# Performance work log

Measured on AMD Instinct MI355X. Metric: run time of the kernel, lower is better.

The kernel has to match this reference:

```python
import jax, jax.numpy as jnp
import numpy as np

N = 100000      # num zones (nodes)
E = 1600000     # num edges
IN = 16         # in_channels
HID = 128       # hidden_dim
HEADS = 4
C = HID // HEADS  # 32, per-head channels of gat1
NEG = 0.2       # PyG GATConv negative_slope default
LN_EPS = 1e-5


def setup_inputs() -> dict:
    key = jax.random.key(0)
    ks = jax.random.split(key, 14)
    x = jax.random.normal(ks[0], (N, IN), jnp.float32)
    edge_index = jax.random.randint(ks[1], (2, E), 0, N, dtype=jnp.int32)
    # --- GATConv layer 1: in=IN, heads=HEADS, out=C, concat=True ---
    W1 = jax.random.normal(ks[2], (IN, HEADS * C), jnp.float32) / np.sqrt(IN)
    a_src1 = jax.random.normal(ks[3], (HEADS, C), jnp.float32) / np.sqrt(C)
    a_dst1 = jax.random.normal(ks[4], (HEADS, C), jnp.float32) / np.sqrt(C)
    b1 = jnp.zeros((HEADS * C,), jnp.float32)
    # --- LayerNorm 1 ---
    g1 = jnp.ones((HID,), jnp.float32)
    beta1 = jnp.zeros((HID,), jnp.float32)
    # --- GATConv layer 2: in=HID, heads=1, out=HID, concat=False ---
    W2 = jax.random.normal(ks[5], (HID, HID), jnp.float32) / np.sqrt(HID)
    a_src2 = jax.random.normal(ks[6], (1, HID), jnp.float32) / np.sqrt(HID)
    a_dst2 = jax.random.normal(ks[7], (1, HID), jnp.float32) / np.sqrt(HID)
    b2 = jnp.zeros((HID,), jnp.float32)
    # --- LayerNorm 2 ---
    g2 = jnp.ones((HID,), jnp.float32)
    beta2 = jnp.zeros((HID,), jnp.float32)
    return dict(x=x, edge_index=edge_index, W1=W1, a_src1=a_src1, a_dst1=a_dst1,
                b1=b1, g1=g1, beta1=beta1, W2=W2, a_src2=a_src2, a_dst2=a_dst2,
                b2=b2, g2=g2, beta2=beta2)


def gat_conv(x, src, dst, W, a_src, a_dst, b, heads, ch, concat):
    """PyG GATConv (eval mode, no edge_attr), self-loops already in src/dst."""
    n = x.shape[0]
    h = (x @ W).reshape(n, heads, ch)                    # [N,H,C]
    alpha_src = jnp.einsum('nhc,hc->nh', h, a_src)       # [N,H]
    alpha_dst = jnp.einsum('nhc,hc->nh', h, a_dst)       # [N,H]
    e = jax.nn.leaky_relu(alpha_src[src] + alpha_dst[dst], NEG)  # [Etot,H]
    # segment softmax over destination node
    m = jax.ops.segment_max(e, dst, num_segments=n)      # [N,H]
    ex = jnp.exp(e - m[dst])
    denom = jax.ops.segment_sum(ex, dst, num_segments=n) # [N,H]
    alpha = ex / denom[dst]                              # [Etot,H]
    msg = h[src] * alpha[..., None]                      # [Etot,H,C]
    out = jax.ops.segment_sum(msg, dst, num_segments=n)  # [N,H,C]
    out = out.reshape(n, heads * ch) if concat else out.mean(axis=1)
    return out + b


def layer_norm(x, g, b):
    mu = x.mean(-1, keepdims=True)
    var = ((x - mu) ** 2).mean(-1, keepdims=True)
    return (x - mu) * jax.lax.rsqrt(var + LN_EPS) * g + b


def reference(x, edge_index, W1, a_src1, a_dst1, b1, g1, beta1,
              W2, a_src2, a_dst2, b2, g2, beta2):
    loops = jnp.arange(N, dtype=edge_index.dtype)
    src = jnp.concatenate([edge_index[0], loops])
    dst = jnp.concatenate([edge_index[1], loops])
    h = gat_conv(x, src, dst, W1, a_src1, a_dst1, b1, HEADS, C, concat=True)
    h = layer_norm(jax.nn.elu(h), g1, beta1)
    h = gat_conv(h, src, dst, W2, a_src2, a_dst2, b2, 1, HID, concat=False)
    h = layer_norm(jax.nn.elu(h), g2, beta2)
    return h
```

## Files before the change

### kernel.cpp

```cpp
#include <hip/hip_runtime.h>

#define IN_CH 16
#define HID 128
#define HEADS 4
#define NEG 0.2f
#define LN_EPS 1e-5f
#define BCAP 8192

typedef short bf16x8 __attribute__((ext_vector_type(8)));
typedef float f32x4 __attribute__((ext_vector_type(4)));

__device__ __forceinline__ float bf2f(unsigned short u) {
  return __uint_as_float(((unsigned)u) << 16);
}
__device__ __forceinline__ float bflo(unsigned u) {
  return __uint_as_float(u << 16);
}
__device__ __forceinline__ float bfhi(unsigned u) {
  return __uint_as_float(u & 0xffff0000u);
}
__device__ __forceinline__ unsigned short f2bf(float f) {
  unsigned u = __float_as_uint(f);
  unsigned r = (u + 0x7fffu + ((u >> 16) & 1u)) >> 16;
  return (unsigned short)r;
}
__device__ __forceinline__ float sb(unsigned v, int sh) {
  return (float)((int)(v << (24 - sh)) >> 24);
}

__global__ __launch_bounds__(256) void k_gemm1(
    const float* __restrict__ x, const float* __restrict__ W1,
    const float* __restrict__ a_src, const float* __restrict__ a_dst,
    signed char* __restrict__ hq, float* __restrict__ rec,
    float* __restrict__ adst, int N) {
  __shared__ float w1s[IN_CH][HID];
  __shared__ float xsh[8][IN_CH];
  int tid = threadIdx.x;
  int nb = blockIdx.x * 8;
  for (int i = tid; i < IN_CH * HID; i += 256) ((float*)w1s)[i] = W1[i];
  if (tid < 128) {
    int nl = tid >> 4, k = tid & 15;
    int n = nb + nl;
    xsh[nl][k] = (n < N) ? x[n * IN_CH + k] : 0.f;
  }
  __syncthreads();
  int nl = tid >> 5;
  int l32 = tid & 31;
  int c0 = l32 << 2;
  int n = nb + nl;
  float4 acc = make_float4(0.f, 0.f, 0.f, 0.f);
#pragma unroll
  for (int k = 0; k < IN_CH; ++k) {
    float xv = xsh[nl][k];
    float4 wv = *(const float4*)(&w1s[k][c0]);
    acc.x += xv * wv.x;
    acc.y += xv * wv.y;
    acc.z += xv * wv.z;
    acc.w += xv * wv.w;
  }
  float4 as4 = *(const float4*)(a_src + c0);
  float4 ad4 = *(const float4*)(a_dst + c0);
  float av = acc.x * as4.x + acc.y * as4.y + acc.z * as4.z + acc.w * as4.w;
  float dv = acc.x * ad4.x + acc.y * ad4.y + acc.z * ad4.z + acc.w * ad4.w;
  av += __shfl_xor(av, 1);
  av += __shfl_xor(av, 2);
  av += __shfl_xor(av, 4);
  dv += __shfl_xor(dv, 1);
  dv += __shfl_xor(dv, 2);
  dv += __shfl_xor(dv, 4);
  float m = fmaxf(fmaxf(fabsf(acc.x), fabsf(acc.y)),
                  fmaxf(fabsf(acc.z), fabsf(acc.w)));
#pragma unroll
  for (int o = 1; o < 32; o <<= 1) m = fmaxf(m, __shfl_xor(m, o));
  if (n < N) {
    float rs = (m > 0.f) ? 127.f / m : 0.f;
    int b0 = __float2int_rn(acc.x * rs) & 255;
    int b1 = __float2int_rn(acc.y * rs) & 255;
    int b2 = __float2int_rn(acc.z * rs) & 255;
    int b3 = __float2int_rn(acc.w * rs) & 255;
    *(unsigned*)(hq + (size_t)n * HID + c0) =
        (unsigned)(b0 | (b1 << 8) | (b2 << 16) | (b3 << 24));
    if ((l32 & 7) == 0) {
      rec[n * 8 + (l32 >> 3)] = av;
      adst[n * HEADS + (l32 >> 3)] = dv;
    }
    if (l32 == 0) rec[n * 8 + 4] = m * (1.f / 127.f);
  }
}

__global__ __launch_bounds__(256) void k_hist(
    const int* __restrict__ ei, int E, int Etot, int NBK, int NBLK,
    int* __restrict__ bcnt) {
  __shared__ int lh[512];
  int blk = blockIdx.x;
  for (int i = threadIdx.x; i < 512; i += 256) lh[i] = 0;
  __syncthreads();
  int s0 = blk * 8192, s1 = min(s0 + 8192, Etot);
  for (int e = s0 + threadIdx.x; e < s1; e += 256) {
    int d = (e < E) ? ei[E + e] : (e - E);
    atomicAdd(&lh[d >> 8], 1);
  }
  __syncthreads();
  for (int i = threadIdx.x; i < NBK; i += 256) bcnt[i * NBLK + blk] = lh[i];
}

__global__ __launch_bounds__(256) void k_scan1(
    const int* __restrict__ deg, int* __restrict__ part, int* __restrict__ aux,
    int N) {
  int i = blockIdx.x * 256 + threadIdx.x;
  int v = (i < N) ? deg[i] : 0;
  int lane = threadIdx.x & 63, w = threadIdx.x >> 6;
  int inc = v;
#pragma unroll
  for (int o = 1; o < 64; o <<= 1) {
    int t = __shfl_up(inc, o, 64);
    if (lane >= o) inc += t;
  }
  __shared__ int wsum[4];
  if (lane == 63) wsum[w] = inc;
  __syncthreads();
  int woff = 0;
#pragma unroll
  for (int k = 0; k < 4; ++k)
    if (k < w) woff += wsum[k];
  if (i < N) part[i] = woff + inc - v;
  if (threadIdx.x == 255) aux[blockIdx.x] = woff + inc;
}

__global__ __launch_bounds__(512) void k_scan2(int* __restrict__ aux, int nb) {
  int i = threadIdx.x;
  int v = (i < nb) ? aux[i] : 0;
  int lane = i & 63, w = i >> 6;
  int inc = v;
#pragma unroll
  for (int o = 1; o < 64; o <<= 1) {
    int t = __shfl_up(inc, o, 64);
    if (lane >= o) inc += t;
  }
  __shared__ int wsum[8];
  if (lane == 63) wsum[w] = inc;
  __syncthreads();
  int woff = 0;
#pragma unroll
  for (int k = 0; k < 8; ++k)
    if (k < w) woff += wsum[k];
  if (i < nb) aux[i] = woff + inc - v;
}

__global__ __launch_bounds__(256) void k_scan3g(
    const int* __restrict__ part, const int* __restrict__ aux,
    int* __restrict__ out, int M) {
  int i = blockIdx.x * 256 + threadIdx.x;
  if (i < M) out[i] = part[i] + aux[blockIdx.x];
}

__global__ __launch_bounds__(256) void k_bucket(
    const int* __restrict__ ei, const int* __restrict__ bpre, int E, int Etot,
    int NBK, int NBLK, unsigned* __restrict__ bbuf) {
  __shared__ int lc[512];
  int blk = blockIdx.x;
  for (int i = threadIdx.x; i < NBK; i += 256) lc[i] = bpre[i * NBLK + blk];
  __syncthreads();
  int s0 = blk * 8192, s1 = min(s0 + 8192, Etot);
  for (int e = s0 + threadIdx.x; e < s1; e += 256) {
    int d = (e < E) ? ei[E + e] : (e - E);
    int s = (e < E) ? ei[e] : d;
    int pos = atomicAdd(&lc[d >> 8], 1);
    bbuf[pos] = ((unsigned)s << 8) | (unsigned)(d & 255);
  }
}

__global__ __launch_bounds__(256) void k_build(
    const unsigned* __restrict__ bbuf, const int* __restrict__ bpre,
    int* __restrict__ rowstart, int* __restrict__ csr_src, int N, int Etot,
    int NBK, int NBLK) {
  __shared__ int ldeg[256], lcur[256], wsum[4];
  __shared__ int lout[BCAP];
  int bin = blockIdx.x;
  int base = bpre[bin * NBLK];
  int next = (bin + 1 < NBK) ? bpre[(bin + 1) * NBLK] : Etot;
  int cnt = next - base;
  if (cnt > BCAP) cnt = BCAP;
  int tid = threadIdx.x;
  ldeg[tid] = 0;
  __syncthreads();
  for (int i = tid; i < cnt; i += 256)
    atomicAdd(&ldeg[bbuf[base + i] & 255u], 1);
  __syncthreads();
  int v = ldeg[tid];
  int lane = tid & 63, wv = tid >> 6;
  int inc = v;
#pragma unroll
  for (int o = 1; o < 64; o <<= 1) {
    int t = __shfl_up(inc, o, 64);
    if (lane >= o) inc += t;
  }
  if (lane == 63) wsum[wv] = inc;
  __syncthreads();
  int woff = 0;
#pragma unroll
  for (int k = 0; k < 4; ++k)
    if (k < wv) woff += wsum[k];
  int pre = woff + inc - v;
  int node = bin * 256 + tid;
  if (node < N) rowstart[node] = base + pre;
  lcur[tid] = pre;
  __syncthreads();
  for (int i = tid; i < cnt; i += 256) {
    unsigned u = bbuf[base + i];
    int p = atomicAdd(&lcur[u & 255u], 1);
    lout[p] = (int)(u >> 8);
  }
  __syncthreads();
  for (int i = tid; i < cnt; i += 256) csr_src[base + i] = lout[i];
  if (bin == 0 && tid == 0) rowstart[N] = Etot;
}

__global__ __launch_bounds__(256) void k_agg1(
    const int* __restrict__ rowstart, const int* __restrict__ csr_src,
    const float* __restrict__ rec, const float* __restrict__ adst,
    const signed char* __restrict__ hq, const float* __restrict__ bias,
    const float* __restrict__ g, const float* __restrict__ beta,
    unsigned short* __restrict__ outb, int N) {
  int d = blockIdx.x * 16 + (threadIdx.x >> 4);
  if (d >= N) return;
  int lane = threadIdx.x & 15;
  int c0 = lane << 3;
  int hd = lane >> 2;
  float ad = adst[d * HEADS + hd];
  int beg = rowstart[d], end = rowstart[d + 1];
  float a0 = 0.f, a1 = 0.f, a2 = 0.f, a3 = 0.f;
  float a4 = 0.f, a5 = 0.f, a6 = 0.f, a7 = 0.f, wsum = 0.f;
  for (int i = beg; i < end; i += 8) {
    int s[8];
#pragma unroll
    for (int j = 0; j < 8; ++j) {
      int e = i + j;
      s[j] = csr_src[e < end ? e : end - 1];
    }
    float lg[8], sc[8];
    uint2 p[8];
#pragma unroll
    for (int j = 0; j < 8; ++j) {
      lg[j] = rec[s[j] * 8 + hd];
      sc[j] = rec[s[j] * 8 + 4];
    }
#pragma unroll
    for (int j = 0; j < 8; ++j)
      p[j] = *(const uint2*)(hq + (size_t)s[j] * HID + c0);
#pragma unroll
    for (int j = 0; j < 8; ++j) {
      float v = lg[j] + ad;
      v = v < 0.f ? NEG * v : v;
      float ex = __expf(v);
      float w = (i + j < end) ? ex : 0.f;
      wsum += w;
      float ws = w * sc[j];
      a0 += ws * sb(p[j].x, 0);
      a1 += ws * sb(p[j].x, 8);
      a2 += ws * sb(p[j].x, 16);
      a3 += ws * sb(p[j].x, 24);
      a4 += ws * sb(p[j].y, 0);
      a5 += ws * sb(p[j].y, 8);
      a6 += ws * sb(p[j].y, 16);
      a7 += ws * sb(p[j].y, 24);
    }
  }
  float rw = 1.f / wsum;
  float v0 = a0 * rw + bias[c0 + 0];
  float v1 = a1 * rw + bias[c0 + 1];
  float v2 = a2 * rw + bias[c0 + 2];
  float v3 = a3 * rw + bias[c0 + 3];
  float v4 = a4 * rw + bias[c0 + 4];
  float v5 = a5 * rw + bias[c0 + 5];
  float v6 = a6 * rw + bias[c0 + 6];
  float v7 = a7 * rw + bias[c0 + 7];
  v0 = v0 > 0.f ? v0 : (__expf(v0) - 1.f);
  v1 = v1 > 0.f ? v1 : (__expf(v1) - 1.f);
  v2 = v2 > 0.f ? v2 : (__expf(v2) - 1.f);
  v3 = v3 > 0.f ? v3 : (__expf(v3) - 1.f);
  v4 = v4 > 0.f ? v4 : (__expf(v4) - 1.f);
  v5 = v5 > 0.f ? v5 : (__expf(v5) - 1.f);
  v6 = v6 > 0.f ? v6 : (__expf(v6) - 1.f);
  v7 = v7 > 0.f ? v7 : (__expf(v7) - 1.f);
  float s1 = ((v0 + v1) + (v2 + v3)) + ((v4 + v5) + (v6 + v7));
  float s2 = ((v0 * v0 + v1 * v1) + (v2 * v2 + v3 * v3)) +
             ((v4 * v4 + v5 * v5) + (v6 * v6 + v7 * v7));
#pragma unroll
  for (int o = 8; o > 0; o >>= 1) {
    s1 += __shfl_down(s1, o, 16);
    s2 += __shfl_down(s2, o, 16);
  }
  s1 = __shfl(s1, 0, 16);
  s2 = __shfl(s2, 0, 16);
  float mu = s1 * (1.f / HID);
  float var = s2 * (1.f / HID) - mu * mu;
  float inv = rsqrtf(var + LN_EPS);
  ushort4 q0, q1;
  q0.x = f2bf((v0 - mu) * inv * g[c0 + 0] + beta[c0 + 0]);
  q0.y = f2bf((v1 - mu) * inv * g[c0 + 1] + beta[c0 + 1]);
  q0.z = f2bf((v2 - mu) * inv * g[c0 + 2] + beta[c0 + 2]);
  q0.w = f2bf((v3 - mu) * inv * g[c0 + 3] + beta[c0 + 3]);
  q1.x = f2bf((v4 - mu) * inv * g[c0 + 4] + beta[c0 + 4]);
  q1.y = f2bf((v5 - mu) * inv * g[c0 + 5] + beta[c0 + 5]);
  q1.z = f2bf((v6 - mu) * inv * g[c0 + 6] + beta[c0 + 6]);
  q1.w = f2bf((v7 - mu) * inv * g[c0 + 7] + beta[c0 + 7]);
  *(ushort4*)(outb + (size_t)d * HID + c0) = q0;
  *(ushort4*)(outb + (size_t)d * HID + c0 + 4) = q1;
}

__global__ __launch_bounds__(256) void k_agg2(
    const int* __restrict__ rowstart, const int* __restrict__ csr_src,
    const float2* __restrict__ rec2, const float* __restrict__ adst,
    const signed char* __restrict__ hq2, const float* __restrict__ bias,
    const float* __restrict__ g, const float* __restrict__ beta,
    float* __restrict__ out, int N) {
  int d = blockIdx.x * 16 + (threadIdx.x >> 4);
  if (d >= N) return;
  int lane = threadIdx.x & 15;
  int c0 = lane << 3;
  float ad = adst[d];
  int beg = rowstart[d], end = rowstart[d + 1];
  float a0 = 0.f, a1 = 0.f, a2 = 0.f, a3 = 0.f;
  float a4 = 0.f, a5 = 0.f, a6 = 0.f, a7 = 0.f, wsum = 0.f;
  for (int i = beg; i < end; i += 8) {
    int s[8];
#pragma unroll
    for (int j = 0; j < 8; ++j) {
      int e = i + j;
      s[j] = csr_src[e < end ? e : end - 1];
    }
    float2 r[8];
    uint2 p[8];
#pragma unroll
    for (int j = 0; j < 8; ++j) r[j] = rec2[s[j]];
#pragma unroll
    for (int j = 0; j < 8; ++j)
      p[j] = *(const uint2*)(hq2 + (size_t)s[j] * HID + c0);
#pragma unroll
    for (int j = 0; j < 8; ++j) {
      float v = r[j].x + ad;
      v = v < 0.f ? NEG * v : v;
      float ex = __expf(v);
      float w = (i + j < end) ? ex : 0.f;
      wsum += w;
      float ws = w * r[j].y;
      a0 += ws * sb(p[j].x, 0);
      a1 += ws * sb(p[j].x, 8);
      a2 += ws * sb(p[j].x, 16);
      a3 += ws * sb(p[j].x, 24);
      a4 += ws * sb(p[j].y, 0);
      a5 += ws * sb(p[j].y, 8);
      a6 += ws * sb(p[j].y, 16);
      a7 += ws * sb(p[j].y, 24);
    }
  }
  float rw = 1.f / wsum;
  float v0 = a0 * rw + bias[c0 + 0];
  float v1 = a1 * rw + bias[c0 + 1];
  float v2 = a2 * rw + bias[c0 + 2];
  float v3 = a3 * rw + bias[c0 + 3];
  float v4 = a4 * rw + bias[c0 + 4];
  float v5 = a5 * rw + bias[c0 + 5];
  float v6 = a6 * rw + bias[c0 + 6];
  float v7 = a7 * rw + bias[c0 + 7];
  v0 = v0 > 0.f ? v0 : (__expf(v0) - 1.f);
  v1 = v1 > 0.f ? v1 : (__expf(v1) - 1.f);
  v2 = v2 > 0.f ? v2 : (__expf(v2) - 1.f);
  v3 = v3 > 0.f ? v3 : (__expf(v3) - 1.f);
  v4 = v4 > 0.f ? v4 : (__expf(v4) - 1.f);
  v5 = v5 > 0.f ? v5 : (__expf(v5) - 1.f);
  v6 = v6 > 0.f ? v6 : (__expf(v6) - 1.f);
  v7 = v7 > 0.f ? v7 : (__expf(v7) - 1.f);
  float s1 = ((v0 + v1) + (v2 + v3)) + ((v4 + v5) + (v6 + v7));
  float s2 = ((v0 * v0 + v1 * v1) + (v2 * v2 + v3 * v3)) +
             ((v4 * v4 + v5 * v5) + (v6 * v6 + v7 * v7));
#pragma unroll
  for (int o = 8; o > 0; o >>= 1) {
    s1 += __shfl_down(s1, o, 16);
    s2 += __shfl_down(s2, o, 16);
  }
  s1 = __shfl(s1, 0, 16);
  s2 = __shfl(s2, 0, 16);
  float mu = s1 * (1.f / HID);
  float var = s2 * (1.f / HID) - mu * mu;
  float inv = rsqrtf(var + LN_EPS);
  float4 o0, o1;
  o0.x = (v0 - mu) * inv * g[c0 + 0] + beta[c0 + 0];
  o0.y = (v1 - mu) * inv * g[c0 + 1] + beta[c0 + 1];
  o0.z = (v2 - mu) * inv * g[c0 + 2] + beta[c0 + 2];
  o0.w = (v3 - mu) * inv * g[c0 + 3] + beta[c0 + 3];
  o1.x = (v4 - mu) * inv * g[c0 + 4] + beta[c0 + 4];
  o1.y = (v5 - mu) * inv * g[c0 + 5] + beta[c0 + 5];
  o1.z = (v6 - mu) * inv * g[c0 + 6] + beta[c0 + 6];
  o1.w = (v7 - mu) * inv * g[c0 + 7] + beta[c0 + 7];
  *(float4*)(out + (size_t)d * HID + c0) = o0;
  *(float4*)(out + (size_t)d * HID + c0 + 4) = o1;
}

__global__ __launch_bounds__(256) void k_w2pack(
    const float* __restrict__ W2, unsigned short* __restrict__ w2hi,
    unsigned short* __restrict__ w2lo) {
  int idx = blockIdx.x * 256 + threadIdx.x;
  int i = idx & 7;
  int lane = (idx >> 3) & 63;
  int t = (idx >> 9) & 7;
  int kb = idx >> 12;
  int k = kb * 32 + (lane >> 4) * 8 + i;
  int c = t * 16 + (lane & 15);
  float w = W2[k * HID + c];
  unsigned short hi = f2bf(w);
  float res = w - bf2f(hi);
  w2hi[idx] = hi;
  w2lo[idx] = f2bf(res);
}

__global__ __launch_bounds__(256) void k_gemm2m(
    const unsigned short* __restrict__ x2b,
    const unsigned short* __restrict__ w2hi,
    const unsigned short* __restrict__ w2lo,
    const float* __restrict__ a_src, const float* __restrict__ a_dst,
    signed char* __restrict__ hq2, float2* __restrict__ rec2,
    float* __restrict__ adst, int N) {
  __shared__ float cs[4][16][132];
  int w = threadIdx.x >> 6;
  int l = threadIdx.x & 63;
  int n0 = blockIdx.x * 128 + w * 32;
  int m = l & 15;
  int kg = l >> 4;
  int naA = n0 + m;
  if (naA >= N) naA = N - 1;
  int naB = n0 + 16 + m;
  if (naB >= N) naB = N - 1;
  const unsigned short* xA = x2b + (size_t)naA * HID + kg * 8;
  const unsigned short* xB = x2b + (size_t)naB * HID + kg * 8;
  f32x4 accA[8] = {};
  f32x4 accB[8] = {};
#pragma unroll
  for (int kb = 0; kb < 4; ++kb) {
    bf16x8 aA = *(const bf16x8*)(xA + kb * 32);
    bf16x8 aB = *(const bf16x8*)(xB + kb * 32);
#pragma unroll
    for (int t = 0; t < 8; ++t) {
      bf16x8 bl = *(const bf16x8*)(w2lo + ((kb * 8 + t) * 64 + l) * 8);
      bf16x8 bh = *(const bf16x8*)(w2hi + ((kb * 8 + t) * 64 + l) * 8);
      accA[t] = __builtin_amdgcn_mfma_f32_16x16x32_bf16(aA, bl, accA[t], 0, 0, 0);
      accA[t] = __builtin_amdgcn_mfma_f32_16x16x32_bf16(aA, bh, accA[t], 0, 0, 0);
      accB[t] = __builtin_amdgcn_mfma_f32_16x16x32_bf16(aB, bl, accB[t], 0, 0, 0);
      accB[t] = __builtin_amdgcn_mfma_f32_16x16x32_bf16(aB, bh, accB[t], 0, 0, 0);
    }
  }
  auto epilog = [&](const f32x4(&acc)[8], int noff) {
#pragma unroll
    for (int t = 0; t < 8; ++t)
#pragma unroll
      for (int j = 0; j < 4; ++j) cs[w][kg * 4 + j][t * 16 + m] = acc[t][j];
    __syncthreads();
    int r2 = l & 15;
    int q = l >> 4;
    int n = n0 + noff + r2;
    const float* rowp = &cs[w][r2][0];
    float4 v[8];
    float pa = 0.f, pd = 0.f, mx = 0.f;
#pragma unroll
    for (int j = 0; j < 8; ++j) {
      int cc = q * 32 + j * 4;
      v[j] = *(const float4*)(rowp + cc);
      float4 as = *(const float4*)(a_src + cc);
      float4 av = *(const float4*)(a_dst + cc);
      pa += v[j].x * as.x + v[j].y * as.y + v[j].z * as.z + v[j].w * as.w;
      pd += v[j].x * av.x + v[j].y * av.y + v[j].z * av.z + v[j].w * av.w;
      mx = fmaxf(mx, fmaxf(fmaxf(fabsf(v[j].x), fabsf(v[j].y)),
                           fmaxf(fabsf(v[j].z), fabsf(v[j].w))));
    }
    pa += __shfl_xor(pa, 16);
    pa += __shfl_xor(pa, 32);
    pd += __shfl_xor(pd, 16);
    pd += __shfl_xor(pd, 32);
    mx = fmaxf(mx, __shfl_xor(mx, 16));
    mx = fmaxf(mx, __shfl_xor(mx, 32));
    if (n < N) {
      float rs = (mx > 0.f) ? 127.f / mx : 0.f;
      unsigned u[8];
#pragma unroll
      for (int j = 0; j < 8; ++j) {
        int b0 = __float2int_rn(v[j].x * rs) & 255;
        int b1 = __float2int_rn(v[j].y * rs) & 255;
        int b2 = __float2int_rn(v[j].z * rs) & 255;
        int b3 = __float2int_rn(v[j].w * rs) & 255;
        u[j] = (unsigned)(b0 | (b1 << 8) | (b2 << 16) | (b3 << 24));
      }
      *(uint4*)(hq2 + (size_t)n * HID + q * 32) =
          make_uint4(u[0], u[1], u[2], u[3]);
      *(uint4*)(hq2 + (size_t)n * HID + q * 32 + 16) =
          make_uint4(u[4], u[5], u[6], u[7]);
      if (q == 0) {
        rec2[n] = make_float2(pa, mx * (1.f / 127.f));
        adst[n] = pd;
      }
    }
    __syncthreads();
  };
  epilog(accA, 0);
  epilog(accB, 16);
}

extern "C" void kernel_launch(void* const* d_in, const int* in_sizes, int n_in,
                              void* d_out, int out_size, void* d_ws, size_t ws_size,
                              hipStream_t stream) {
  const float* x      = (const float*)d_in[0];
  const int*   ei     = (const int*)d_in[1];
  const float* W1     = (const float*)d_in[2];
  const float* a_src1 = (const float*)d_in[3];
  const float* a_dst1 = (const float*)d_in[4];
  const float* b1     = (const float*)d_in[5];
  const float* g1     = (const float*)d_in[6];
  const float* beta1  = (const float*)d_in[7];
  const float* W2     = (const float*)d_in[8];
  const float* a_src2 = (const float*)d_in[9];
  const float* a_dst2 = (const float*)d_in[10];
  const float* b2     = (const float*)d_in[11];
  const float* g2     = (const float*)d_in[12];
  const float* beta2  = (const float*)d_in[13];
  float* out = (float*)d_out;

  const int N = in_sizes[0] / IN_CH;
  const int E = in_sizes[1] / 2;
  const int Etot = E + N;

  const int NBK = (N + 255) >> 8;
  const int NBLK = (Etot + 8191) >> 13;
  const int M = NBK * NBLK;
  const int Mblk = (M + 255) / 256;

  unsigned char* U = (unsigned char*)d_ws;
  signed char* hq = (signed char*)U;
  float* rec = (float*)(U + (size_t)N * HID);
  unsigned short* x2b =
      (unsigned short*)(U + (size_t)N * HID + (size_t)N * 32);
  signed char* hq2 = (signed char*)(x2b + (size_t)N * HID);
  float2* rec2 = (float2*)(hq2 + (size_t)N * HID);
  float* adst1 = (float*)(rec2 + N);
  float* adst2 = adst1 + (size_t)N * HEADS;
  int* rowstart = (int*)(adst2 + N);
  int* aux      = rowstart + N + 4;
  int* bcnt     = aux + 1024;
  int* bpart    = bcnt + M;
  int* bpre     = bpart + M;
  unsigned* bbuf = (unsigned*)(bpre + M);
  int* csr_src  = (int*)(bbuf + Etot);
  unsigned short* w2hi = (unsigned short*)(csr_src + Etot);
  unsigned short* w2lo = w2hi + 16384;

  k_w2pack<<<64, 256, 0, stream>>>(W2, w2hi, w2lo);

  k_hist<<<NBLK, 256, 0, stream>>>(ei, E, Etot, NBK, NBLK, bcnt);
  k_scan1<<<Mblk, 256, 0, stream>>>(bcnt, bpart, aux, M);
  k_scan2<<<1, 512, 0, stream>>>(aux, Mblk);
  k_scan3g<<<Mblk, 256, 0, stream>>>(bpart, aux, bpre, M);
  k_bucket<<<NBLK, 256, 0, stream>>>(ei, bpre, E, Etot, NBK, NBLK, bbuf);
  k_build<<<NBK, 256, 0, stream>>>(bbuf, bpre, rowstart, csr_src, N, Etot,
                                   NBK, NBLK);

  k_gemm1<<<(N + 7) / 8, 256, 0, stream>>>(x, W1, a_src1, a_dst1, hq, rec,
                                           adst1, N);
  k_agg1<<<(N + 15) / 16, 256, 0, stream>>>(rowstart, csr_src, rec, adst1, hq,
                                            b1, g1, beta1, x2b, N);

  k_gemm2m<<<(N + 127) / 128, 256, 0, stream>>>(x2b, w2hi, w2lo, a_src2,
                                                a_dst2, hq2, rec2, adst2, N);
  k_agg2<<<(N + 15) / 16, 256, 0, stream>>>(rowstart, csr_src, rec2, adst2,
                                            hq2, b2, g2, beta2, out, N);
}
```

Before: 304.9 us.

## Sort destination nodes by degree to balance aggregation work; pack per-head attention records

After: 311.7 us. 2.2% more time.

```diff
diff --git a/kernel.cpp b/kernel.cpp
--- a/kernel.cpp
+++ b/kernel.cpp
@@ -6,18 +6,13 @@
 #define NEG 0.2f
 #define LN_EPS 1e-5f
 #define BCAP 8192
+#define DB 64
 
 typedef short bf16x8 __attribute__((ext_vector_type(8)));
 typedef float f32x4 __attribute__((ext_vector_type(4)));
 
 __device__ __forceinline__ float bf2f(unsigned short u) {
   return __uint_as_float(((unsigned)u) << 16);
-}
-__device__ __forceinline__ float bflo(unsigned u) {
-  return __uint_as_float(u << 16);
-}
-__device__ __forceinline__ float bfhi(unsigned u) {
-  return __uint_as_float(u & 0xffff0000u);
 }
 __device__ __forceinline__ unsigned short f2bf(float f) {
   unsigned u = __float_as_uint(f);
@@ -31,7 +26,7 @@
 __global__ __launch_bounds__(256) void k_gemm1(
     const float* __restrict__ x, const float* __restrict__ W1,
     const float* __restrict__ a_src, const float* __restrict__ a_dst,
-    signed char* __restrict__ hq, float* __restrict__ rec,
+    signed char* __restrict__ hq, float2* __restrict__ rec1h,
     float* __restrict__ adst, int N) {
   __shared__ float w1s[IN_CH][HID];
   __shared__ float xsh[8][IN_CH];
@@ -81,10 +76,9 @@
     *(unsigned*)(hq + (size_t)n * HID + c0) =
         (unsigned)(b0 | (b1 << 8) | (b2 << 16) | (b3 << 24));
     if ((l32 & 7) == 0) {
-      rec[n * 8 + (l32 >> 3)] = av;
+      rec1h[n * 4 + (l32 >> 3)] = make_float2(av, m * (1.f / 127.f));
       adst[n * HEADS + (l32 >> 3)] = dv;
     }
-    if (l32 == 0) rec[n * 8 + 4] = m * (1.f / 127.f);
   }
 }
 
@@ -172,9 +166,9 @@
 
 __global__ __launch_bounds__(256) void k_build(
     const unsigned* __restrict__ bbuf, const int* __restrict__ bpre,
-    int* __restrict__ rowstart, int* __restrict__ csr_src, int N, int Etot,
-    int NBK, int NBLK) {
-  __shared__ int ldeg[256], lcur[256], wsum[4];
+    int* __restrict__ rowstart, int* __restrict__ csr_src,
+    int* __restrict__ dcnt, int N, int Etot, int NBK, int NBLK) {
+  __shared__ int ldeg[256], lcur[256], wsum[4], ldh[DB];
   __shared__ int lout[BCAP];
   int bin = blockIdx.x;
   int base = bpre[bin * NBLK];
@@ -183,6 +177,7 @@
   if (cnt > BCAP) cnt = BCAP;
   int tid = threadIdx.x;
   ldeg[tid] = 0;
+  if (tid < DB) ldh[tid] = 0;
   __syncthreads();
   for (int i = tid; i < cnt; i += 256)
     atomicAdd(&ldeg[bbuf[base + i] & 255u], 1);
@@ -203,7 +198,10 @@
     if (k < wv) woff += wsum[k];
   int pre = woff + inc - v;
   int node = bin * 256 + tid;
-  if (node < N) rowstart[node] = base + pre;
+  if (node < N) {
+    rowstart[node] = base + pre;
+    atomicAdd(&ldh[min(v, DB - 1)], 1);
+  }
   lcur[tid] = pre;
   __syncthreads();
   for (int i = tid; i < cnt; i += 256) {
@@ -213,17 +211,36 @@
   }
   __syncthreads();
   for (int i = tid; i < cnt; i += 256) csr_src[base + i] = lout[i];
+  if (tid < DB) dcnt[tid * NBK + bin] = ldh[tid];
   if (bin == 0 && tid == 0) rowstart[N] = Etot;
 }
 
+__global__ __launch_bounds__(256) void k_dplace(
+    const int* __restrict__ rowstart, const int* __restrict__ dpre, int N,
+    int NBK, int* __restrict__ perm) {
+  __shared__ int lc[DB];
+  int blk = blockIdx.x;
+  int tid = threadIdx.x;
+  if (tid < DB) lc[tid] = dpre[tid * NBK + blk];
+  __syncthreads();
+  int n = blk * 256 + tid;
+  if (n < N) {
+    int deg = rowstart[n + 1] - rowstart[n];
+    int b = min(deg, DB - 1);
+    int pos = atomicAdd(&lc[b], 1);
+    perm[pos] = n;
+  }
+}
+
 __global__ __launch_bounds__(256) void k_agg1(
-    const int* __restrict__ rowstart, const int* __restrict__ csr_src,
-    const float* __restrict__ rec, const float* __restrict__ adst,
-    const signed char* __restrict__ hq, const float* __restrict__ bias,
-    const float* __restrict__ g, const float* __restrict__ beta,
-    unsigned short* __restrict__ outb, int N) {
-  int d = blockIdx.x * 16 + (threadIdx.x >> 4);
-  if (d >= N) return;
+    const int* __restrict__ perm, const int* __restrict__ rowstart,
+    const int* __restrict__ csr_src, const float2* __restrict__ rec1h,
+    const float* __restrict__ adst, const signed char* __restrict__ hq,
+    const float* __restrict__ bias, const float* __restrict__ g,
+    const float* __restrict__ beta, unsigned short* __restrict__ outb, int N) {
+  int gid = blockIdx.x * 16 + (threadIdx.x >> 4);
+  if (gid >= N) return;
+  int d = perm[gid];
   int lane = threadIdx.x & 15;
   int c0 = lane << 3;
   int hd = lane >> 2;
@@ -238,24 +255,21 @@
       int e = i + j;
       s[j] = csr_src[e < end ? e : end - 1];
     }
-    float lg[8], sc[8];
+    float2 r[8];
     uint2 p[8];
 #pragma unroll
-    for (int j = 0; j < 8; ++j) {
-      lg[j] = rec[s[j] * 8 + hd];
-      sc[j] = rec[s[j] * 8 + 4];
-    }
+    for (int j = 0; j < 8; ++j) r[j] = rec1h[s[j] * 4 + hd];
 #pragma unroll
     for (int j = 0; j < 8; ++j)
       p[j] = *(const uint2*)(hq + (size_t)s[j] * HID + c0);
 #pragma unroll
     for (int j = 0; j < 8; ++j) {
-      float v = lg[j] + ad;
+      float v = r[j].x + ad;
       v = v < 0.f ? NEG * v : v;
       float ex = __expf(v);
       float w = (i + j < end) ? ex : 0.f;
       wsum += w;
-      float ws = w * sc[j];
+      float ws = w * r[j].y;
       a0 += ws * sb(p[j].x, 0);
       a1 += ws * sb(p[j].x, 8);
       a2 += ws * sb(p[j].x, 16);
@@ -310,13 +324,14 @@
 }
 
 __global__ __launch_bounds__(256) void k_agg2(
-    const int* __restrict__ rowstart, const int* __restrict__ csr_src,
-    const float2* __restrict__ rec2, const float* __restrict__ adst,
-    const signed char* __restrict__ hq2, const float* __restrict__ bias,
-    const float* __restrict__ g, const float* __restrict__ beta,
-    float* __restrict__ out, int N) {
-  int d = blockIdx.x * 16 + (threadIdx.x >> 4);
-  if (d >= N) return;
+    const int* __restrict__ perm, const int* __restrict__ rowstart,
+    const int* __restrict__ csr_src, const float2* __restrict__ rec2,
+    const float* __restrict__ adst, const signed char* __restrict__ hq2,
+    const float* __restrict__ bias, const float* __restrict__ g,
+    const float* __restrict__ beta, float* __restrict__ out, int N) {
+  int gid = blockIdx.x * 16 + (threadIdx.x >> 4);
+  if (gid >= N) return;
+  int d = perm[gid];
   int lane = threadIdx.x & 15;
   int c0 = lane << 3;
   float ad = adst[d];
@@ -532,10 +547,12 @@
   const int NBLK = (Etot + 8191) >> 13;
   const int M = NBK * NBLK;
   const int Mblk = (M + 255) / 256;
+  const int M2 = DB * NBK;
+  const int M2blk = (M2 + 255) / 256;
 
   unsigned char* U = (unsigned char*)d_ws;
   signed char* hq = (signed char*)U;
-  float* rec = (float*)(U + (size_t)N * HID);
+  float2* rec1h = (float2*)(U + (size_t)N * HID);
   unsigned short* x2b =
       (unsigned short*)(U + (size_t)N * HID + (size_t)N * 32);
   signed char* hq2 = (signed char*)(x2b + (size_t)N * HID);
@@ -551,6 +568,7 @@
   int* csr_src  = (int*)(bbuf + Etot);
   unsigned short* w2hi = (unsigned short*)(csr_src + Etot);
   unsigned short* w2lo = w2hi + 16384;
+  int* perm = (int*)(w2lo + 16384);
 
   k_w2pack<<<64, 256, 0, stream>>>(W2, w2hi, w2lo);
 
@@ -559,16 +577,21 @@
   k_scan2<<<1, 512, 0, stream>>>(aux, Mblk);
   k_scan3g<<<Mblk, 256, 0, stream>>>(bpart, aux, bpre, M);
   k_bucket<<<NBLK, 256, 0, stream>>>(ei, bpre, E, Etot, NBK, NBLK, bbuf);
-  k_build<<<NBK, 256, 0, stream>>>(bbuf, bpre, rowstart, csr_src, N, Etot,
-                                   NBK, NBLK);
-
-  k_gemm1<<<(N + 7) / 8, 256, 0, stream>>>(x, W1, a_src1, a_dst1, hq, rec,
+  k_build<<<NBK, 256, 0, stream>>>(bbuf, bpre, rowstart, csr_src, bcnt, N,
+                                   Etot, NBK, NBLK);
+
+  k_scan1<<<M2blk, 256, 0, stream>>>(bcnt, bpart, aux, M2);
+  k_scan2<<<1, 512, 0, stream>>>(aux, M2blk);
+  k_scan3g<<<M2blk, 256, 0, stream>>>(bpart, aux, bpre, M2);
+  k_dplace<<<NBK, 256, 0, stream>>>(rowstart, bpre, N, NBK, perm);
+
+  k_gemm1<<<(N + 7) / 8, 256, 0, stream>>>(x, W1, a_src1, a_dst1, hq, rec1h,
                                            adst1, N);
-  k_agg1<<<(N + 15) / 16, 256, 0, stream>>>(rowstart, csr_src, rec, adst1, hq,
-                                            b1, g1, beta1, x2b, N);
+  k_agg1<<<(N + 15) / 16, 256, 0, stream>>>(perm, rowstart, csr_src, rec1h,
+                                            adst1, hq, b1, g1, beta1, x2b, N);
 
   k_gemm2m<<<(N + 127) / 128, 256, 0, stream>>>(x2b, w2hi, w2lo, a_src2,
                                                 a_dst2, hq2, rec2, adst2, N);
-  k_agg2<<<(N + 15) / 16, 256, 0, stream>>>(rowstart, csr_src, rec2, adst2,
-                                            hq2, b2, g2, beta2, out, N);
-}
+  k_agg2<<<(N + 15) / 16, 256, 0, stream>>>(perm, rowstart, csr_src, rec2,
+                                            adst2, hq2, b2, g2, beta2, out, N);
+}
```
